# Kernel tuning notes

Hardware: AMD Instinct MI355X
Metric: run time of the kernel (lower is better)

The kernel has to match this reference:

```python
import jax, jax.numpy as jnp
import numpy as np

NUM_EMBEDDINGS = 512
EMBEDDING_DIM = 64
COMMITMENT_SCALAR = 0.25


def setup_inputs() -> dict:
    key = jax.random.key(0)
    k_in, k_emb = jax.random.split(key)
    inputs = jax.random.normal(k_in, (64, 4096, EMBEDDING_DIM), dtype=jnp.float32)
    # nn.Embedding weight, init U(-1/K, 1/K) as in the torch module
    emb_weight = jax.random.uniform(
        k_emb, (NUM_EMBEDDINGS, EMBEDDING_DIM), dtype=jnp.float32,
        minval=-1.0 / NUM_EMBEDDINGS, maxval=1.0 / NUM_EMBEDDINGS)
    return {"inputs": inputs, "emb_weight": emb_weight}


def reference(inputs, emb_weight):
    input_shape = inputs.shape
    flat = inputs.reshape(-1, EMBEDDING_DIM)  # [N, D]
    distances = (jnp.sum(flat ** 2, axis=1, keepdims=True)
                 + jnp.sum(emb_weight ** 2, axis=1)
                 - 2.0 * flat @ emb_weight.T)
    encoding_indices = jnp.argmin(distances, axis=1)  # [N]
    # one-hot @ codebook == gather of codebook rows
    quantized = emb_weight[encoding_indices].reshape(input_shape)
    e_latent_loss = jnp.mean((jax.lax.stop_gradient(quantized) - inputs) ** 2)
    q_latent_loss = jnp.mean((quantized - jax.lax.stop_gradient(inputs)) ** 2)
    loss = q_latent_loss + COMMITMENT_SCALAR * e_latent_loss
    # straight-through estimator (training mode)
    quantized = inputs + jax.lax.stop_gradient(quantized - inputs)
    return encoding_indices[:, None], quantized, loss
```

## Files before the change

kernel.cpp:

```cpp
#include <hip/hip_runtime.h>


#define NROWS (64 * 4096)
#define DIMS 64
#define KCODES 512
#define BLOCK 512
#define ROWS_PER_BLOCK 1024
#define GRID (NROWS / ROWS_PER_BLOCK)
#define CBS 17

struct Lds {
  float4 cb[KCODES * CBS];
  float  bf[KCODES];
  int    kidx[ROWS_PER_BLOCK];
  double red[8];
};

__device__ __forceinline__ float pairwise64_sq(const float4* v) {
  float a[64];
  #pragma unroll
  for (int c = 0; c < 16; ++c) {
    a[4 * c + 0] = v[c].x * v[c].x;
    a[4 * c + 1] = v[c].y * v[c].y;
    a[4 * c + 2] = v[c].z * v[c].z;
    a[4 * c + 3] = v[c].w * v[c].w;
  }
  float r0 = a[0], r1 = a[1], r2 = a[2], r3 = a[3];
  float r4 = a[4], r5 = a[5], r6 = a[6], r7 = a[7];
  #pragma unroll
  for (int i = 8; i < 64; i += 8) {
    r0 += a[i + 0]; r1 += a[i + 1]; r2 += a[i + 2]; r3 += a[i + 3];
    r4 += a[i + 4]; r5 += a[i + 5]; r6 += a[i + 6]; r7 += a[i + 7];
  }
  return ((r0 + r1) + (r2 + r3)) + ((r4 + r5) + (r6 + r7));
}

__global__ __launch_bounds__(BLOCK, 2) void vq_main(
    const float* __restrict__ x, const float* __restrict__ emb,
    float* __restrict__ out_idx, float* __restrict__ out_q,
    double* __restrict__ ws) {
  __shared__ Lds L;
  const int tid = threadIdx.x;
  const int row0 = blockIdx.x * ROWS_PER_BLOCK;

  const float4* emb4 = (const float4*)emb;
  #pragma unroll
  for (int i = 0; i < 16; ++i) {
    int f = tid + i * BLOCK;
    int k = f >> 4, c = f & 15;
    L.cb[k * CBS + c] = emb4[f];
  }
  {
    float4 er[16];
    const float4* p = emb4 + tid * 16;
    #pragma unroll
    for (int c = 0; c < 16; ++c) er[c] = p[c];
    L.bf[tid] = pairwise64_sq(er);
  }

  const int rA = row0 + tid;
  const int rB = rA + BLOCK;
  float4 xv[16], yv[16];
  {
    const float4* pa = (const float4*)(x + (size_t)rA * DIMS);
    const float4* pb = (const float4*)(x + (size_t)rB * DIMS);
    #pragma unroll
    for (int c = 0; c < 16; ++c) { xv[c] = pa[c]; yv[c] = pb[c]; }
  }
  const float s1A = pairwise64_sq(xv);
  const float s1B = pairwise64_sq(yv);

  __syncthreads();

  float d1A = 3.4e38f, d1B = 3.4e38f;
  int kA = 0, kB = 0;
  #pragma unroll 2
  for (int k = 0; k < KCODES; ++k) {
    const float4* e = &L.cb[k * CBS];
    float accA = 0.f, accB = 0.f;
    #pragma unroll
    for (int c = 0; c < 16; ++c) {
      float4 ev = e[c];
      float4 xc = xv[c];
      float4 yc = yv[c];
      accA = fmaf(xc.x, ev.x, accA);
      accA = fmaf(xc.y, ev.y, accA);
      accA = fmaf(xc.z, ev.z, accA);
      accA = fmaf(xc.w, ev.w, accA);
      accB = fmaf(yc.x, ev.x, accB);
      accB = fmaf(yc.y, ev.y, accB);
      accB = fmaf(yc.z, ev.z, accB);
      accB = fmaf(yc.w, ev.w, accB);
    }
    float bk = L.bf[k];
    float SA = s1A + bk;
    float SB = s1B + bk;
    float dA = SA - 2.0f * accA;
    float dB = SB - 2.0f * accB;
    if (dA < d1A) { d1A = dA; kA = k; }
    if (dB < d1B) { d1B = dB; kB = k; }
  }

  double lsum = 0.0;
  {
    const float4* ea = &L.cb[kA * CBS];
    const float4* eb = &L.cb[kB * CBS];
    #pragma unroll
    for (int c = 0; c < 16; ++c) {
      float4 va = ea[c], vb = eb[c];
      float4 xc = xv[c], yc = yv[c];
      float a0 = va.x - xc.x, a1 = va.y - xc.y, a2 = va.z - xc.z, a3 = va.w - xc.w;
      float c0 = vb.x - yc.x, c1 = vb.y - yc.y, c2 = vb.z - yc.z, c3 = vb.w - yc.w;
      lsum += (double)a0 * a0 + (double)a1 * a1 + (double)a2 * a2 + (double)a3 * a3;
      lsum += (double)c0 * c0 + (double)c1 * c1 + (double)c2 * c2 + (double)c3 * c3;
    }
  }

  out_idx[rA] = (float)kA;
  out_idx[rB] = (float)kB;
  L.kidx[tid] = kA;
  L.kidx[tid + BLOCK] = kB;

  #pragma unroll
  for (int off = 32; off > 0; off >>= 1) lsum += __shfl_down(lsum, off);
  if ((tid & 63) == 0) L.red[tid >> 6] = lsum;

  __syncthreads();

  if (tid == 0) {
    double s = 0.0;
    #pragma unroll
    for (int w = 0; w < 8; ++w) s += L.red[w];
    ws[blockIdx.x] = s;
  }

  float4* outq4 = (float4*)out_q;
  #pragma unroll
  for (int it = 0; it < 32; ++it) {
    int idx = it * BLOCK + tid;
    int r = idx >> 4, c = idx & 15;
    float4 v = L.cb[L.kidx[r] * CBS + c];
    outq4[(size_t)(row0 + r) * 16 + c] = v;
  }
}

__global__ void vq_loss_finalize(const double* __restrict__ ws,
                                 float* __restrict__ out_loss) {
  double s = 0.0;
  for (int i = threadIdx.x; i < GRID; i += 64) s += ws[i];
  #pragma unroll
  for (int off = 32; off > 0; off >>= 1) s += __shfl_down(s, off);
  if (threadIdx.x == 0)
    *out_loss = (float)(1.25 * s / (double)((size_t)NROWS * DIMS));
}

extern "C" void kernel_launch(void* const* d_in, const int* in_sizes, int n_in,
                              void* d_out, int out_size, void* d_ws, size_t ws_size,
                              hipStream_t stream) {
  (void)in_sizes; (void)n_in; (void)out_size; (void)ws_size;
  const float* x   = (const float*)d_in[0];
  const float* emb = (const float*)d_in[1];
  float* out      = (float*)d_out;
  float* out_idx  = out;
  float* out_q    = out + NROWS;
  float* out_loss = out + NROWS + (size_t)NROWS * DIMS;
  double* ws = (double*)d_ws;

  vq_main<<<GRID, BLOCK, 0, stream>>>(x, emb, out_idx, out_q, ws);
  vq_loss_finalize<<<1, 64, 0, stream>>>(ws, out_loss);
}
```

Measured before the change: 304.7 us.

## Stream codebook via scalar loads instead of LDS, one row per thread

The codebook is no longer staged in LDS. Each iteration loads the wave-uniform codebook row and its squared norm into SGPRs with inline s_load_dwordx16, so the FMAs take scalar operands and skip the LDS read traffic. Codebook norms now come from a small separate kernel. The loss is taken from the minimum distance itself rather than recomputing the squared difference against the chosen code. The block shrinks to 256 threads with one row each, and the quantized output is gathered from global memory; the price is a scalar-load wait on every iteration and lower float precision in the loss value.

Result: slower. 319.3 us (+4.8%).

```diff
diff --git a/kernel.cpp b/kernel.cpp
--- a/kernel.cpp
+++ b/kernel.cpp
@@ -4,17 +4,12 @@
 #define NROWS (64 * 4096)
 #define DIMS 64
 #define KCODES 512
-#define BLOCK 512
-#define ROWS_PER_BLOCK 1024
-#define GRID (NROWS / ROWS_PER_BLOCK)
-#define CBS 17
+#define BLOCK 256
+#define GRID (NROWS / BLOCK)
+#define WS_S2_OFF 0
+#define WS_RED_OFF 4096
 
-struct Lds {
-  float4 cb[KCODES * CBS];
-  float  bf[KCODES];
-  int    kidx[ROWS_PER_BLOCK];
-  double red[8];
-};
+typedef unsigned int u16v __attribute__((ext_vector_type(16)));
 
 __device__ __forceinline__ float pairwise64_sq(const float4* v) {
   float a[64];
@@ -35,112 +30,93 @@
   return ((r0 + r1) + (r2 + r3)) + ((r4 + r5) + (r6 + r7));
 }
 
-__global__ __launch_bounds__(BLOCK, 2) void vq_main(
+__global__ void vq_s2(const float* __restrict__ emb, float* __restrict__ s2) {
+  int k = blockIdx.x * 256 + threadIdx.x;
+  const float4* row = (const float4*)(emb + (size_t)k * DIMS);
+  float4 r[16];
+  #pragma unroll
+  for (int c = 0; c < 16; ++c) r[c] = row[c];
+  s2[k] = pairwise64_sq(r);
+}
+
+#define FMA4(E, j0, c)                                        \
+  acc = fmaf(xv[c].x, __uint_as_float(E[(j0) + 0]), acc);     \
+  acc = fmaf(xv[c].y, __uint_as_float(E[(j0) + 1]), acc);     \
+  acc = fmaf(xv[c].z, __uint_as_float(E[(j0) + 2]), acc);     \
+  acc = fmaf(xv[c].w, __uint_as_float(E[(j0) + 3]), acc);
+
+__global__ __launch_bounds__(BLOCK) void vq_main(
     const float* __restrict__ x, const float* __restrict__ emb,
-    float* __restrict__ out_idx, float* __restrict__ out_q,
-    double* __restrict__ ws) {
-  __shared__ Lds L;
+    const float* __restrict__ s2, float* __restrict__ out_idx,
+    float* __restrict__ out_q, double* __restrict__ ws) {
+  __shared__ int   kidx[BLOCK];
+  __shared__ double red[BLOCK / 64];
   const int tid = threadIdx.x;
-  const int row0 = blockIdx.x * ROWS_PER_BLOCK;
+  const int row0 = blockIdx.x * BLOCK;
+  const int r = row0 + tid;
 
-  const float4* emb4 = (const float4*)emb;
-  #pragma unroll
-  for (int i = 0; i < 16; ++i) {
-    int f = tid + i * BLOCK;
-    int k = f >> 4, c = f & 15;
-    L.cb[k * CBS + c] = emb4[f];
+  float4 xv[16];
+  {
+    const float4* p = (const float4*)(x + (size_t)r * DIMS);
+    #pragma unroll
+    for (int c = 0; c < 16; ++c) xv[c] = p[c];
   }
-  {
-    float4 er[16];
-    const float4* p = emb4 + tid * 16;
-    #pragma unroll
-    for (int c = 0; c < 16; ++c) er[c] = p[c];
-    L.bf[tid] = pairwise64_sq(er);
+  const float s1 = pairwise64_sq(xv);
+
+  float d1 = 3.4e38f;
+  int kbest = 0;
+  #pragma unroll 1
+  for (int k = 0; k < KCODES; ++k) {
+    const float* pe = emb + (size_t)k * DIMS;
+    const float* ps = s2 + k;
+    u16v e0, e1, e2, e3;
+    unsigned int bku;
+    asm volatile(
+        "s_load_dwordx16 %0, %5, 0x0\n\t"
+        "s_load_dwordx16 %1, %5, 0x40\n\t"
+        "s_load_dwordx16 %2, %5, 0x80\n\t"
+        "s_load_dwordx16 %3, %5, 0xc0\n\t"
+        "s_load_dword    %4, %6, 0x0\n\t"
+        "s_waitcnt lgkmcnt(0)"
+        : "=&s"(e0), "=&s"(e1), "=&s"(e2), "=&s"(e3), "=&s"(bku)
+        : "s"(pe), "s"(ps));
+
+    float acc = 0.f;
+    FMA4(e0,  0, 0)  FMA4(e0,  4, 1)  FMA4(e0,  8, 2)  FMA4(e0, 12, 3)
+    FMA4(e1,  0, 4)  FMA4(e1,  4, 5)  FMA4(e1,  8, 6)  FMA4(e1, 12, 7)
+    FMA4(e2,  0, 8)  FMA4(e2,  4, 9)  FMA4(e2,  8, 10) FMA4(e2, 12, 11)
+    FMA4(e3,  0, 12) FMA4(e3,  4, 13) FMA4(e3,  8, 14) FMA4(e3, 12, 15)
+
+    float S = s1 + __uint_as_float(bku);
+    float d = fmaf(-2.0f, acc, S);
+    if (d < d1) { d1 = d; kbest = k; }
   }
 
-  const int rA = row0 + tid;
-  const int rB = rA + BLOCK;
-  float4 xv[16], yv[16];
-  {
-    const float4* pa = (const float4*)(x + (size_t)rA * DIMS);
-    const float4* pb = (const float4*)(x + (size_t)rB * DIMS);
-    #pragma unroll
-    for (int c = 0; c < 16; ++c) { xv[c] = pa[c]; yv[c] = pb[c]; }
-  }
-  const float s1A = pairwise64_sq(xv);
-  const float s1B = pairwise64_sq(yv);
+  out_idx[r] = (float)kbest;
+  kidx[tid] = kbest;
 
-  __syncthreads();
-
-  float d1A = 3.4e38f, d1B = 3.4e38f;
-  int kA = 0, kB = 0;
-  #pragma unroll 2
-  for (int k = 0; k < KCODES; ++k) {
-    const float4* e = &L.cb[k * CBS];
-    float accA = 0.f, accB = 0.f;
-    #pragma unroll
-    for (int c = 0; c < 16; ++c) {
-      float4 ev = e[c];
-      float4 xc = xv[c];
-      float4 yc = yv[c];
-      accA = fmaf(xc.x, ev.x, accA);
-      accA = fmaf(xc.y, ev.y, accA);
-      accA = fmaf(xc.z, ev.z, accA);
-      accA = fmaf(xc.w, ev.w, accA);
-      accB = fmaf(yc.x, ev.x, accB);
-      accB = fmaf(yc.y, ev.y, accB);
-      accB = fmaf(yc.z, ev.z, accB);
-      accB = fmaf(yc.w, ev.w, accB);
-    }
-    float bk = L.bf[k];
-    float SA = s1A + bk;
-    float SB = s1B + bk;
-    float dA = SA - 2.0f * accA;
-    float dB = SB - 2.0f * accB;
-    if (dA < d1A) { d1A = dA; kA = k; }
-    if (dB < d1B) { d1B = dB; kB = k; }
-  }
-
-  double lsum = 0.0;
-  {
-    const float4* ea = &L.cb[kA * CBS];
-    const float4* eb = &L.cb[kB * CBS];
-    #pragma unroll
-    for (int c = 0; c < 16; ++c) {
-      float4 va = ea[c], vb = eb[c];
-      float4 xc = xv[c], yc = yv[c];
-      float a0 = va.x - xc.x, a1 = va.y - xc.y, a2 = va.z - xc.z, a3 = va.w - xc.w;
-      float c0 = vb.x - yc.x, c1 = vb.y - yc.y, c2 = vb.z - yc.z, c3 = vb.w - yc.w;
-      lsum += (double)a0 * a0 + (double)a1 * a1 + (double)a2 * a2 + (double)a3 * a3;
-      lsum += (double)c0 * c0 + (double)c1 * c1 + (double)c2 * c2 + (double)c3 * c3;
-    }
-  }
-
-  out_idx[rA] = (float)kA;
-  out_idx[rB] = (float)kB;
-  L.kidx[tid] = kA;
-  L.kidx[tid + BLOCK] = kB;
-
+  double lsum = (double)d1;
   #pragma unroll
   for (int off = 32; off > 0; off >>= 1) lsum += __shfl_down(lsum, off);
-  if ((tid & 63) == 0) L.red[tid >> 6] = lsum;
+  if ((tid & 63) == 0) red[tid >> 6] = lsum;
 
   __syncthreads();
 
   if (tid == 0) {
     double s = 0.0;
     #pragma unroll
-    for (int w = 0; w < 8; ++w) s += L.red[w];
+    for (int w = 0; w < BLOCK / 64; ++w) s += red[w];
     ws[blockIdx.x] = s;
   }
 
+  const float4* emb4 = (const float4*)emb;
   float4* outq4 = (float4*)out_q;
   #pragma unroll
-  for (int it = 0; it < 32; ++it) {
+  for (int it = 0; it < 16; ++it) {
     int idx = it * BLOCK + tid;
-    int r = idx >> 4, c = idx & 15;
-    float4 v = L.cb[L.kidx[r] * CBS + c];
-    outq4[(size_t)(row0 + r) * 16 + c] = v;
+    int rr = idx >> 4, c = idx & 15;
+    float4 v = emb4[(size_t)kidx[rr] * 16 + c];
+    outq4[(size_t)(row0 + rr) * 16 + c] = v;
   }
 }
 
@@ -164,8 +140,10 @@
   float* out_idx  = out;
   float* out_q    = out + NROWS;
   float* out_loss = out + NROWS + (size_t)NROWS * DIMS;
-  double* ws = (double*)d_ws;
+  float*  ws_s2  = (float*)((char*)d_ws + WS_S2_OFF);
+  double* ws_red = (double*)((char*)d_ws + WS_RED_OFF);
 
-  vq_main<<<GRID, BLOCK, 0, stream>>>(x, emb, out_idx, out_q, ws);
-  vq_loss_finalize<<<1, 64, 0, stream>>>(ws, out_loss);
+  vq_s2<<<2, 256, 0, stream>>>(emb, ws_s2);
+  vq_main<<<GRID, BLOCK, 0, stream>>>(x, emb, ws_s2, out_idx, out_q, ws_red);
+  vq_loss_finalize<<<1, 64, 0, stream>>>(ws_red, out_loss);
 }
```
